# Kernel tuning notes

Measured on AMD Instinct MI355X. Metric: run time of the kernel, lower is better.

Reference implementation:

```python
import jax, jax.numpy as jnp
import numpy as np

N_NODES = 50000
N_GRAPHS = 64


def gcn_conv(x, W, b, src, dst, n_nodes):
    # PyG GCNConv: add self-loops, symmetric normalization D^-1/2 A D^-1/2,
    # linear transform, scatter-sum aggregation from src -> dst, plus bias.
    si = jnp.arange(n_nodes, dtype=src.dtype)
    s = jnp.concatenate([src, si])
    d = jnp.concatenate([dst, si])
    deg = jax.ops.segment_sum(jnp.ones_like(d, dtype=x.dtype), d, num_segments=n_nodes)
    dinv = jax.lax.rsqrt(jnp.maximum(deg, 1.0))  # deg >= 1 due to self-loops
    norm = dinv[s] * dinv[d]                      # [E+N]
    h = x @ W                                     # [N, out]
    msg = h[s] * norm[:, None]                    # gather + scale
    out = jax.ops.segment_sum(msg, d, num_segments=n_nodes)
    return out + b


def setup_inputs() -> dict:
    key = jax.random.key(0)
    ks = jax.random.split(key, 12)
    input_dim, hidden, half = 128, 64, 32
    x = jax.random.normal(ks[0], (N_NODES, input_dim), dtype=jnp.float32)
    edge_index = jax.random.randint(ks[1], (2, 800000), 0, N_NODES, dtype=jnp.int64)
    batch = jnp.sort(jax.random.randint(ks[2], (N_NODES,), 0, N_GRAPHS, dtype=jnp.int64))
    def lin(k, fan_in, fan_out):
        s = 1.0 / np.sqrt(fan_in)
        return jax.random.uniform(k, (fan_in, fan_out), jnp.float32, -s, s)
    return {
        "x": x,
        "edge_index": edge_index,
        "batch": batch,
        "W1": lin(ks[3], input_dim, hidden), "b1": jnp.zeros((hidden,), jnp.float32),
        "W2": lin(ks[4], hidden, hidden),    "b2": jnp.zeros((hidden,), jnp.float32),
        "Wc1": lin(ks[5], hidden, half),     "bc1": jnp.zeros((half,), jnp.float32),
        "Wc2": lin(ks[6], half, 1),          "bc2": jnp.zeros((1,), jnp.float32),
    }


def reference(x, edge_index, batch, W1, b1, W2, b2, Wc1, bc1, Wc2, bc2):
    src, dst = edge_index[0], edge_index[1]
    h = jax.nn.relu(gcn_conv(x, W1, b1, src, dst, N_NODES))
    # F.dropout(training=False) -> identity in eval
    h = jax.nn.relu(gcn_conv(h, W2, b2, src, dst, N_NODES))
    # global_mean_pool over graphs
    sums = jax.ops.segment_sum(h, batch, num_segments=N_GRAPHS)
    cnts = jax.ops.segment_sum(jnp.ones((h.shape[0], 1), h.dtype), batch, num_segments=N_GRAPHS)
    g = sums / jnp.maximum(cnts, 1.0)             # [G, hidden]
    # MLP head (Dropout(0.2) is identity in eval)
    z = jax.nn.relu(g @ Wc1 + bc1)
    return z @ Wc2 + bc2                          # [G, 1]
```

## Files before the change

### kernel.cpp

```cpp
#include <hip/hip_runtime.h>
#include <math.h>

#define NG 64
#define HID 64

typedef __attribute__((ext_vector_type(8))) short bf16x8;
typedef __attribute__((ext_vector_type(4))) float f32x4;

__device__ __forceinline__ unsigned int bfbits(float f) {
    unsigned int u = __float_as_uint(f);
    return (u + 0x7FFFu + ((u >> 16) & 1u)) >> 16;
}
__device__ __forceinline__ float bfval(unsigned int bits) {
    return __uint_as_float(bits << 16);
}

__global__ void k_deg(const int* __restrict__ dst, int E,
                      int* __restrict__ deg, int* __restrict__ rank) {
    int i = blockIdx.x * blockDim.x + threadIdx.x;
    if (i < E) rank[i] = atomicAdd(deg + dst[i], 1);
}

__global__ __launch_bounds__(256) void k_scan1(const int* __restrict__ deg,
                                               int* __restrict__ excl,
                                               int* __restrict__ bsum,
                                               float* __restrict__ dinv, int n) {
    __shared__ int tmp[256];
    int b = blockIdx.x, t = threadIdx.x;
    int base = b * 1024 + t * 4;
    int v[4];
#pragma unroll
    for (int j = 0; j < 4; ++j) v[j] = (base + j < n) ? deg[base + j] : 0;
#pragma unroll
    for (int j = 0; j < 4; ++j)
        if (base + j < n) dinv[base + j] = 1.0f / sqrtf((float)v[j] + 1.0f);
    int s = v[0] + v[1] + v[2] + v[3];
    tmp[t] = s;
    __syncthreads();
    for (int off = 1; off < 256; off <<= 1) {
        int x = (t >= off) ? tmp[t - off] : 0;
        __syncthreads();
        tmp[t] += x;
        __syncthreads();
    }
    int run = tmp[t] - s;
#pragma unroll
    for (int j = 0; j < 4; ++j) {
        if (base + j < n) excl[base + j] = run;
        run += v[j];
    }
    if (t == 255) bsum[b] = tmp[255];
}

__global__ __launch_bounds__(256) void k_scan23(const int* __restrict__ excl,
                                                const int* __restrict__ bsum,
                                                const int* __restrict__ batch,
                                                int* __restrict__ rowstart,
                                                int* __restrict__ gstart,
                                                int n, int E, int nb) {
    __shared__ int bs[256];
    __shared__ int pre;
    const int t = threadIdx.x;
    if (t < nb) bs[t] = bsum[t];
    __syncthreads();
    if (t == 0) {
        int seg = (blockIdx.x * 256) >> 10;
        int s = 0;
        for (int b = 0; b < seg; ++b) s += bs[b];
        pre = s;
    }
    __syncthreads();
    int i = blockIdx.x * 256 + t;
    if (i < n) {
        rowstart[i] = excl[i] + pre;
        int bi = batch[i];
        int bp = (i == 0) ? -1 : batch[i - 1];
        for (int g = bp + 1; g <= bi; ++g) gstart[g] = i;
        if (i == n - 1)
            for (int g = bi + 1; g <= NG; ++g) gstart[g] = n;
    }
    if (i == 0) rowstart[n] = E;
}

__global__ void k_fill(const int* __restrict__ src, const int* __restrict__ dst,
                       const int* __restrict__ rank, const int* __restrict__ rowstart,
                       int* __restrict__ col, int E) {
    int e = blockIdx.x * blockDim.x + threadIdx.x;
    if (e >= E) return;
    col[rowstart[dst[e]] + rank[e]] = src[e];
}

__global__ void k_wconv(const float* __restrict__ W1, const float* __restrict__ W2,
                        unsigned short* __restrict__ W1hi, unsigned short* __restrict__ W1lo,
                        unsigned short* __restrict__ W2hi, unsigned short* __restrict__ W2lo) {
    int i = blockIdx.x * blockDim.x + threadIdx.x;
    if (i < 128 * 64) {
        int k = i >> 6, c = i & 63;
        float f = W1[i];
        unsigned hb = bfbits(f);
        W1hi[c * 128 + k] = (unsigned short)hb;
        W1lo[c * 128 + k] = (unsigned short)bfbits(f - bfval(hb));
    }
    int i2 = i - 128 * 64;
    if (i2 >= 0 && i2 < 64 * 64) {
        int k = i2 >> 6, c = i2 & 63;
        float f = W2[i2];
        unsigned hb = bfbits(f);
        W2hi[c * 64 + k] = (unsigned short)hb;
        W2lo[c * 64 + k] = (unsigned short)bfbits(f - bfval(hb));
    }
}

template<int K>
__global__ __launch_bounds__(256) void k_gemm_mfma(const float* __restrict__ A,
                                                   const unsigned short* __restrict__ Whi,
                                                   const unsigned short* __restrict__ Wlo,
                                                   const float* __restrict__ dinv,
                                                   float* __restrict__ out, int n) {
    const int wave = threadIdx.x >> 6, lane = threadIdx.x & 63;
    const int ntile2 = (n + 31) >> 5;
    const int tile2 = blockIdx.x * 4 + wave;
    if (tile2 >= ntile2) return;
    const int lrow = lane & 15;
    const int kgrp = lane >> 4;
    const int r0 = tile2 * 32 + lrow;
    const int r1 = r0 + 16;

    f32x4 acc0[4], acc1[4];
#pragma unroll
    for (int ct = 0; ct < 4; ++ct) {
        acc0[ct] = (f32x4){0.f, 0.f, 0.f, 0.f};
        acc1[ct] = (f32x4){0.f, 0.f, 0.f, 0.f};
    }

#pragma unroll
    for (int s = 0; s < K / 32; ++s) {
        float a0[8], a1[8];
        {
            const float* p0 = A + (size_t)r0 * K + s * 32 + kgrp * 8;
            const float* p1 = A + (size_t)r1 * K + s * 32 + kgrp * 8;
            float4 u0, u1, w0, w1;
            if (r0 < n) { u0 = *(const float4*)p0; u1 = *(const float4*)(p0 + 4); }
            else { u0 = make_float4(0.f,0.f,0.f,0.f); u1 = u0; }
            if (r1 < n) { w0 = *(const float4*)p1; w1 = *(const float4*)(p1 + 4); }
            else { w0 = make_float4(0.f,0.f,0.f,0.f); w1 = w0; }
            a0[0]=u0.x; a0[1]=u0.y; a0[2]=u0.z; a0[3]=u0.w;
            a0[4]=u1.x; a0[5]=u1.y; a0[6]=u1.z; a0[7]=u1.w;
            a1[0]=w0.x; a1[1]=w0.y; a1[2]=w0.z; a1[3]=w0.w;
            a1[4]=w1.x; a1[5]=w1.y; a1[6]=w1.z; a1[7]=w1.w;
        }
        bf16x8 ahi0, alo0, ahi1, alo1;
#pragma unroll
        for (int e = 0; e < 8; ++e) {
            unsigned hb0 = bfbits(a0[e]);
            ahi0[e] = (short)hb0;
            alo0[e] = (short)bfbits(a0[e] - bfval(hb0));
            unsigned hb1 = bfbits(a1[e]);
            ahi1[e] = (short)hb1;
            alo1[e] = (short)bfbits(a1[e] - bfval(hb1));
        }
#pragma unroll
        for (int ct = 0; ct < 4; ++ct) {
            const size_t wo = (size_t)(ct * 16 + lrow) * K + s * 32 + kgrp * 8;
            bf16x8 whi = *(const bf16x8*)(Whi + wo);
            bf16x8 wlo = *(const bf16x8*)(Wlo + wo);
            acc0[ct] = __builtin_amdgcn_mfma_f32_16x16x32_bf16(ahi0, whi, acc0[ct], 0, 0, 0);
            acc0[ct] = __builtin_amdgcn_mfma_f32_16x16x32_bf16(alo0, whi, acc0[ct], 0, 0, 0);
            acc0[ct] = __builtin_amdgcn_mfma_f32_16x16x32_bf16(ahi0, wlo, acc0[ct], 0, 0, 0);
            acc1[ct] = __builtin_amdgcn_mfma_f32_16x16x32_bf16(ahi1, whi, acc1[ct], 0, 0, 0);
            acc1[ct] = __builtin_amdgcn_mfma_f32_16x16x32_bf16(alo1, whi, acc1[ct], 0, 0, 0);
            acc1[ct] = __builtin_amdgcn_mfma_f32_16x16x32_bf16(ahi1, wlo, acc1[ct], 0, 0, 0);
        }
    }

#pragma unroll
    for (int r = 0; r < 4; ++r) {
        int o0 = tile2 * 32 + kgrp * 4 + r;
        if (o0 < n) {
            float dv = dinv[o0];
#pragma unroll
            for (int ct = 0; ct < 4; ++ct)
                out[(size_t)o0 * HID + ct * 16 + lrow] = acc0[ct][r] * dv;
        }
        int o1 = o0 + 16;
        if (o1 < n) {
            float dv = dinv[o1];
#pragma unroll
            for (int ct = 0; ct < 4; ++ct)
                out[(size_t)o1 * HID + ct * 16 + lrow] = acc1[ct][r] * dv;
        }
    }
}

__global__ __launch_bounds__(256) void k_gather(const float* __restrict__ hs,
                                                const int* __restrict__ rowstart,
                                                const int* __restrict__ col,
                                                const float* __restrict__ dinv,
                                                const float* __restrict__ bias,
                                                float* __restrict__ out, int n) {
    const int wave = threadIdx.x >> 6, lane = threadIdx.x & 63;
    const int n0 = blockIdx.x * 8 + wave * 2;
    if (n0 >= n) return;
    const int n1 = n0 + 1;
    const bool has1 = (n1 < n);
    const float bl = bias[lane];

    float di0 = dinv[n0];
    float acc0 = hs[(size_t)n0 * HID + lane], acc0b = 0.f;
    int j0 = rowstart[n0], e0 = rowstart[n0 + 1];
    float di1 = 0.f, acc1 = 0.f, acc1b = 0.f;
    int j1 = 0, e1 = 0;
    if (has1) {
        di1 = dinv[n1];
        acc1 = hs[(size_t)n1 * HID + lane];
        j1 = e0;
        e1 = rowstart[n1 + 1];
    }

    while (e0 - j0 >= 8 && e1 - j1 >= 8) {
        const int jb0 = __builtin_amdgcn_readfirstlane(j0);
        const int jb1 = __builtin_amdgcn_readfirstlane(j1);
        int c0[8], c1[8];
#pragma unroll
        for (int t = 0; t < 8; ++t) c0[t] = col[jb0 + t];
#pragma unroll
        for (int t = 0; t < 8; ++t) c1[t] = col[jb1 + t];
        float v0[8], v1[8];
#pragma unroll
        for (int t = 0; t < 8; ++t) v0[t] = hs[(size_t)c0[t] * HID + lane];
#pragma unroll
        for (int t = 0; t < 8; ++t) v1[t] = hs[(size_t)c1[t] * HID + lane];
#pragma unroll
        for (int t = 0; t < 8; ++t) { if (t & 1) acc0b += v0[t]; else acc0 += v0[t]; }
#pragma unroll
        for (int t = 0; t < 8; ++t) { if (t & 1) acc1b += v1[t]; else acc1 += v1[t]; }
        j0 += 8; j1 += 8;
    }
    while (e0 - j0 >= 8) {
        const int jb = __builtin_amdgcn_readfirstlane(j0);
        int c[8];
#pragma unroll
        for (int t = 0; t < 8; ++t) c[t] = col[jb + t];
        float v[8];
#pragma unroll
        for (int t = 0; t < 8; ++t) v[t] = hs[(size_t)c[t] * HID + lane];
#pragma unroll
        for (int t = 0; t < 8; ++t) { if (t & 1) acc0b += v[t]; else acc0 += v[t]; }
        j0 += 8;
    }
    while (e1 - j1 >= 8) {
        const int jb = __builtin_amdgcn_readfirstlane(j1);
        int c[8];
#pragma unroll
        for (int t = 0; t < 8; ++t) c[t] = col[jb + t];
        float v[8];
#pragma unroll
        for (int t = 0; t < 8; ++t) v[t] = hs[(size_t)c[t] * HID + lane];
#pragma unroll
        for (int t = 0; t < 8; ++t) { if (t & 1) acc1b += v[t]; else acc1 += v[t]; }
        j1 += 8;
    }
    for (; j0 + 1 < e0; j0 += 2) {
        acc0  += hs[(size_t)col[j0] * HID + lane];
        acc0b += hs[(size_t)col[j0 + 1] * HID + lane];
    }
    if (j0 < e0) acc0 += hs[(size_t)col[j0] * HID + lane];
    for (; j1 + 1 < e1; j1 += 2) {
        acc1  += hs[(size_t)col[j1] * HID + lane];
        acc1b += hs[(size_t)col[j1 + 1] * HID + lane];
    }
    if (j1 < e1) acc1 += hs[(size_t)col[j1] * HID + lane];

    out[(size_t)n0 * HID + lane] = fmaxf(fmaf(acc0 + acc0b, di0, bl), 0.f);
    if (has1)
        out[(size_t)n1 * HID + lane] = fmaxf(fmaf(acc1 + acc1b, di1, bl), 0.f);
}

__global__ __launch_bounds__(512) void k_poolhead(const float* __restrict__ h,
                                                  const int* __restrict__ gstart,
                                                  const float* __restrict__ Wc1,
                                                  const float* __restrict__ bc1,
                                                  const float* __restrict__ Wc2,
                                                  const float* __restrict__ bc2,
                                                  float* __restrict__ outp, int n) {
    const int g = blockIdx.x;
    const int lo = gstart[g], lo2 = gstart[g + 1];
    const int t = threadIdx.x;
    const int rg = t >> 4;
    const int c4 = (t & 15) * 4;
    float4 acc = make_float4(0.f, 0.f, 0.f, 0.f);
    for (int r = lo + rg; r < lo2; r += 32) {
        float4 v = *(const float4*)(h + (size_t)r * HID + c4);
        acc.x += v.x; acc.y += v.y; acc.z += v.z; acc.w += v.w;
    }
    __shared__ float4 red[32][16];
    __shared__ float gmv[HID];
    __shared__ float zs[32];
    red[rg][t & 15] = acc;
    __syncthreads();
    if (t < 16) {
        float4 s = red[0][t];
#pragma unroll
        for (int g2 = 1; g2 < 32; ++g2) {
            float4 v = red[g2][t];
            s.x += v.x; s.y += v.y; s.z += v.z; s.w += v.w;
        }
        float inv = 1.0f / fmaxf((float)(lo2 - lo), 1.0f);
        gmv[t * 4 + 0] = s.x * inv; gmv[t * 4 + 1] = s.y * inv;
        gmv[t * 4 + 2] = s.z * inv; gmv[t * 4 + 3] = s.w * inv;
    }
    __syncthreads();
    if (t < 32) {
        float z = bc1[t];
#pragma unroll 8
        for (int k = 0; k < HID; ++k) z = fmaf(gmv[k], Wc1[k * 32 + t], z);
        zs[t] = fmaxf(z, 0.f) * Wc2[t];
    }
    __syncthreads();
    if (t == 0) {
        float o = bc2[0];
#pragma unroll
        for (int j = 0; j < 32; ++j) o += zs[j];
        outp[g] = o;
    }
}

extern "C" void kernel_launch(void* const* d_in, const int* in_sizes, int n_in,
                              void* d_out, int out_size, void* d_ws, size_t ws_size,
                              hipStream_t stream) {
    const float* x    = (const float*)d_in[0];
    const int*   ei   = (const int*)d_in[1];
    const int*   batch= (const int*)d_in[2];
    const float* W1   = (const float*)d_in[3];
    const float* b1   = (const float*)d_in[4];
    const float* W2   = (const float*)d_in[5];
    const float* b2   = (const float*)d_in[6];
    const float* Wc1  = (const float*)d_in[7];
    const float* bc1  = (const float*)d_in[8];
    const float* Wc2  = (const float*)d_in[9];
    const float* bc2  = (const float*)d_in[10];

    const int E = in_sizes[1] / 2;
    const int n = in_sizes[0] / 128;
    const int* srcp = ei;
    const int* dstp = ei + E;
    const int nb = (n + 1023) / 1024;

    char* ws = (char*)d_ws;
    auto alloc = [&](size_t bytes) {
        char* p = ws;
        ws += (bytes + 255) & ~(size_t)255;
        return p;
    };
    int*   deg      = (int*)  alloc((size_t)n * 4);
    float* dinv     = (float*)alloc((size_t)n * 4);
    int*   excl     = (int*)  alloc((size_t)n * 4);
    int*   bsum     = (int*)  alloc((size_t)nb * 4);
    int*   rowstart = (int*)  alloc((size_t)(n + 1) * 4);
    int*   gstart   = (int*)  alloc((size_t)(NG + 1) * 4);
    int*   rank     = (int*)  alloc((size_t)E * 4);
    int*   col      = (int*)  alloc((size_t)E * 4);
    float* bufA     = (float*)alloc((size_t)n * HID * 4);
    float* bufB     = (float*)alloc((size_t)n * HID * 4);
    unsigned short* W1hi = (unsigned short*)alloc(128 * 64 * 2);
    unsigned short* W1lo = (unsigned short*)alloc(128 * 64 * 2);
    unsigned short* W2hi = (unsigned short*)alloc(64 * 64 * 2);
    unsigned short* W2lo = (unsigned short*)alloc(64 * 64 * 2);

    hipMemsetAsync(deg, 0, (size_t)n * 4, stream);

    k_deg   <<<(E + 255) / 256, 256, 0, stream>>>(dstp, E, deg, rank);
    k_scan1 <<<nb, 256, 0, stream>>>(deg, excl, bsum, dinv, n);
    k_scan23<<<(n + 255) / 256, 256, 0, stream>>>(excl, bsum, batch, rowstart, gstart, n, E, nb);
    k_fill  <<<(E + 255) / 256, 256, 0, stream>>>(srcp, dstp, rank, rowstart, col, E);
    k_wconv <<<(128 * 64 + 64 * 64 + 255) / 256, 256, 0, stream>>>(W1, W2, W1hi, W1lo, W2hi, W2lo);

    const int mblocks = ((n + 31) / 32 + 3) / 4;
    const int gblocks = (n + 7) / 8;

    k_gemm_mfma<128><<<mblocks, 256, 0, stream>>>(x, W1hi, W1lo, dinv, bufA, n);
    k_gather<<<gblocks, 256, 0, stream>>>(bufA, rowstart, col, dinv, b1, bufB, n);

    k_gemm_mfma<64><<<mblocks, 256, 0, stream>>>(bufB, W2hi, W2lo, dinv, bufA, n);
    k_gather<<<gblocks, 256, 0, stream>>>(bufA, rowstart, col, dinv, b2, bufB, n);

    k_poolhead<<<NG, 512, 0, stream>>>(bufB, gstart, Wc1, bc1, Wc2, bc2, (float*)d_out, n);
}
```

Baseline: 169.9 us.

## Fuse layer-1 gather with layer-2 GEMM and merge weight conversion into scan

Adds a kernel that aggregates 32 nodes per block into shared memory, applies bias and ReLU, then runs the 64x64 layer-2 transform with split-bf16 MFMA and dinv scaling directly. This removes one launch and a full N×64 intermediate write and read. The weight hi/lo conversion now runs as extra blocks of the scan23 kernel, removing one more launch. The fused kernel uses 512-thread blocks with a barrier between gather and GEMM, which may reduce latency hiding for the irregular gathers.

```diff
diff --git a/kernel.cpp b/kernel.cpp
--- a/kernel.cpp
+++ b/kernel.cpp
@@ -57,10 +57,34 @@
                                                 const int* __restrict__ batch,
                                                 int* __restrict__ rowstart,
                                                 int* __restrict__ gstart,
-                                                int n, int E, int nb) {
+                                                const float* __restrict__ W1,
+                                                const float* __restrict__ W2,
+                                                unsigned short* __restrict__ W1hi,
+                                                unsigned short* __restrict__ W1lo,
+                                                unsigned short* __restrict__ W2hi,
+                                                unsigned short* __restrict__ W2lo,
+                                                int n, int E, int nb, int nblk) {
+    const int t = threadIdx.x;
+    if (blockIdx.x >= nblk) {
+        int idx = (blockIdx.x - nblk) * 256 + t;
+        if (idx < 128 * 64) {
+            int k = idx >> 6, c = idx & 63;
+            float f = W1[idx];
+            unsigned hb = bfbits(f);
+            W1hi[c * 128 + k] = (unsigned short)hb;
+            W1lo[c * 128 + k] = (unsigned short)bfbits(f - bfval(hb));
+        } else if (idx < 128 * 64 + 64 * 64) {
+            int i2 = idx - 128 * 64;
+            int k = i2 >> 6, c = i2 & 63;
+            float f = W2[i2];
+            unsigned hb = bfbits(f);
+            W2hi[c * 64 + k] = (unsigned short)hb;
+            W2lo[c * 64 + k] = (unsigned short)bfbits(f - bfval(hb));
+        }
+        return;
+    }
     __shared__ int bs[256];
     __shared__ int pre;
-    const int t = threadIdx.x;
     if (t < nb) bs[t] = bsum[t];
     __syncthreads();
     if (t == 0) {
@@ -88,27 +112,6 @@
     int e = blockIdx.x * blockDim.x + threadIdx.x;
     if (e >= E) return;
     col[rowstart[dst[e]] + rank[e]] = src[e];
-}
-
-__global__ void k_wconv(const float* __restrict__ W1, const float* __restrict__ W2,
-                        unsigned short* __restrict__ W1hi, unsigned short* __restrict__ W1lo,
-                        unsigned short* __restrict__ W2hi, unsigned short* __restrict__ W2lo) {
-    int i = blockIdx.x * blockDim.x + threadIdx.x;
-    if (i < 128 * 64) {
-        int k = i >> 6, c = i & 63;
-        float f = W1[i];
-        unsigned hb = bfbits(f);
-        W1hi[c * 128 + k] = (unsigned short)hb;
-        W1lo[c * 128 + k] = (unsigned short)bfbits(f - bfval(hb));
-    }
-    int i2 = i - 128 * 64;
-    if (i2 >= 0 && i2 < 64 * 64) {
-        int k = i2 >> 6, c = i2 & 63;
-        float f = W2[i2];
-        unsigned hb = bfbits(f);
-        W2hi[c * 64 + k] = (unsigned short)hb;
-        W2lo[c * 64 + k] = (unsigned short)bfbits(f - bfval(hb));
-    }
 }
 
 template<int K>
@@ -192,6 +195,128 @@
     }
 }
 
+__global__ __launch_bounds__(512) void k_gather_gemm2(const float* __restrict__ hs,
+                                                      const int* __restrict__ rowstart,
+                                                      const int* __restrict__ col,
+                                                      const float* __restrict__ dinv,
+                                                      const float* __restrict__ bias,
+                                                      const unsigned short* __restrict__ Whi,
+                                                      const unsigned short* __restrict__ Wlo,
+                                                      float* __restrict__ outB, int n) {
+    __shared__ float Ash[32][68];
+    const int wave = threadIdx.x >> 6, lane = threadIdx.x & 63;
+    const int nodebase = blockIdx.x * 32 + wave * 4;
+    const float bl = bias[lane];
+
+#pragma unroll
+    for (int p = 0; p < 2; ++p) {
+        const int n0 = nodebase + 2 * p;
+        const int n1 = n0 + 1;
+        const bool has0 = (n0 < n), has1 = (n1 < n);
+        float di0 = 0.f, acc0 = 0.f, acc0b = 0.f;
+        float di1 = 0.f, acc1 = 0.f, acc1b = 0.f;
+        int j0 = 0, e0 = 0, j1 = 0, e1 = 0;
+        if (has0) {
+            di0 = dinv[n0];
+            acc0 = hs[(size_t)n0 * HID + lane];
+            j0 = rowstart[n0]; e0 = rowstart[n0 + 1];
+        }
+        if (has1) {
+            di1 = dinv[n1];
+            acc1 = hs[(size_t)n1 * HID + lane];
+            j1 = e0; e1 = rowstart[n1 + 1];
+        }
+        while (e0 - j0 >= 8 && e1 - j1 >= 8) {
+            const int jb0 = __builtin_amdgcn_readfirstlane(j0);
+            const int jb1 = __builtin_amdgcn_readfirstlane(j1);
+            int c0[8], c1[8];
+#pragma unroll
+            for (int t = 0; t < 8; ++t) c0[t] = col[jb0 + t];
+#pragma unroll
+            for (int t = 0; t < 8; ++t) c1[t] = col[jb1 + t];
+            float v0[8], v1[8];
+#pragma unroll
+            for (int t = 0; t < 8; ++t) v0[t] = hs[(size_t)c0[t] * HID + lane];
+#pragma unroll
+            for (int t = 0; t < 8; ++t) v1[t] = hs[(size_t)c1[t] * HID + lane];
+#pragma unroll
+            for (int t = 0; t < 8; ++t) { if (t & 1) acc0b += v0[t]; else acc0 += v0[t]; }
+#pragma unroll
+            for (int t = 0; t < 8; ++t) { if (t & 1) acc1b += v1[t]; else acc1 += v1[t]; }
+            j0 += 8; j1 += 8;
+        }
+        while (e0 - j0 >= 8) {
+            const int jb = __builtin_amdgcn_readfirstlane(j0);
+            int c[8];
+#pragma unroll
+            for (int t = 0; t < 8; ++t) c[t] = col[jb + t];
+            float v[8];
+#pragma unroll
+            for (int t = 0; t < 8; ++t) v[t] = hs[(size_t)c[t] * HID + lane];
+#pragma unroll
+            for (int t = 0; t < 8; ++t) { if (t & 1) acc0b += v[t]; else acc0 += v[t]; }
+            j0 += 8;
+        }
+        while (e1 - j1 >= 8) {
+            const int jb = __builtin_amdgcn_readfirstlane(j1);
+            int c[8];
+#pragma unroll
+            for (int t = 0; t < 8; ++t) c[t] = col[jb + t];
+            float v[8];
+#pragma unroll
+            for (int t = 0; t < 8; ++t) v[t] = hs[(size_t)c[t] * HID + lane];
+#pragma unroll
+            for (int t = 0; t < 8; ++t) { if (t & 1) acc1b += v[t]; else acc1 += v[t]; }
+            j1 += 8;
+        }
+        for (; j0 + 1 < e0; j0 += 2) {
+            acc0  += hs[(size_t)col[j0] * HID + lane];
+            acc0b += hs[(size_t)col[j0 + 1] * HID + lane];
+        }
+        if (j0 < e0) acc0 += hs[(size_t)col[j0] * HID + lane];
+        for (; j1 + 1 < e1; j1 += 2) {
+            acc1  += hs[(size_t)col[j1] * HID + lane];
+            acc1b += hs[(size_t)col[j1 + 1] * HID + lane];
+        }
+        if (j1 < e1) acc1 += hs[(size_t)col[j1] * HID + lane];
+
+        Ash[wave * 4 + 2 * p][lane]     = has0 ? fmaxf(fmaf(acc0 + acc0b, di0, bl), 0.f) : 0.f;
+        Ash[wave * 4 + 2 * p + 1][lane] = has1 ? fmaxf(fmaf(acc1 + acc1b, di1, bl), 0.f) : 0.f;
+    }
+    __syncthreads();
+
+    const int rowhalf = wave >> 2, ct = wave & 3;
+    const int lrow = lane & 15;
+    const int kgrp = lane >> 4;
+    f32x4 acc = (f32x4){0.f, 0.f, 0.f, 0.f};
+#pragma unroll
+    for (int s = 0; s < 2; ++s) {
+        const float* ap = &Ash[rowhalf * 16 + lrow][s * 32 + kgrp * 8];
+        float4 u0 = *(const float4*)ap;
+        float4 u1 = *(const float4*)(ap + 4);
+        float av[8] = {u0.x, u0.y, u0.z, u0.w, u1.x, u1.y, u1.z, u1.w};
+        bf16x8 ahi, alo;
+#pragma unroll
+        for (int e = 0; e < 8; ++e) {
+            unsigned hb = bfbits(av[e]);
+            ahi[e] = (short)hb;
+            alo[e] = (short)bfbits(av[e] - bfval(hb));
+        }
+        const size_t wo = (size_t)(ct * 16 + lrow) * 64 + s * 32 + kgrp * 8;
+        bf16x8 whi = *(const bf16x8*)(Whi + wo);
+        bf16x8 wlo = *(const bf16x8*)(Wlo + wo);
+        acc = __builtin_amdgcn_mfma_f32_16x16x32_bf16(ahi, whi, acc, 0, 0, 0);
+        acc = __builtin_amdgcn_mfma_f32_16x16x32_bf16(alo, whi, acc, 0, 0, 0);
+        acc = __builtin_amdgcn_mfma_f32_16x16x32_bf16(ahi, wlo, acc, 0, 0, 0);
+    }
+#pragma unroll
+    for (int r = 0; r < 4; ++r) {
+        int orow = blockIdx.x * 32 + rowhalf * 16 + kgrp * 4 + r;
+        if (orow < n)
+            outB[(size_t)orow * HID + ct * 16 + lrow] = acc[r] * dinv[orow];
+    }
+}
+
 __global__ __launch_bounds__(256) void k_gather(const float* __restrict__ hs,
                                                 const int* __restrict__ rowstart,
                                                 const int* __restrict__ col,
@@ -213,10 +338,8 @@
     if (has1) {
         di1 = dinv[n1];
         acc1 = hs[(size_t)n1 * HID + lane];
-        j1 = e0;
-        e1 = rowstart[n1 + 1];
-    }
-
+        j1 = e0; e1 = rowstart[n1 + 1];
+    }
     while (e0 - j0 >= 8 && e1 - j1 >= 8) {
         const int jb0 = __builtin_amdgcn_readfirstlane(j0);
         const int jb1 = __builtin_amdgcn_readfirstlane(j1);
@@ -369,20 +492,22 @@
 
     hipMemsetAsync(deg, 0, (size_t)n * 4, stream);
 
+    const int nblk = (n + 255) / 256;
+    const int wblk = (128 * 64 + 64 * 64 + 255) / 256;
+
     k_deg   <<<(E + 255) / 256, 256, 0, stream>>>(dstp, E, deg, rank);
     k_scan1 <<<nb, 256, 0, stream>>>(deg, excl, bsum, dinv, n);
-    k_scan23<<<(n + 255) / 256, 256, 0, stream>>>(excl, bsum, batch, rowstart, gstart, n, E, nb);
+    k_scan23<<<nblk + wblk, 256, 0, stream>>>(excl, bsum, batch, rowstart, gstart,
+                                              W1, W2, W1hi, W1lo, W2hi, W2lo,
+                                              n, E, nb, nblk);
     k_fill  <<<(E + 255) / 256, 256, 0, stream>>>(srcp, dstp, rank, rowstart, col, E);
-    k_wconv <<<(128 * 64 + 64 * 64 + 255) / 256, 256, 0, stream>>>(W1, W2, W1hi, W1lo, W2hi, W2lo);
 
     const int mblocks = ((n + 31) / 32 + 3) / 4;
-    const int gblocks = (n + 7) / 8;
 
     k_gemm_mfma<128><<<mblocks, 256, 0, stream>>>(x, W1hi, W1lo, dinv, bufA, n);
-    k_gather<<<gblocks, 256, 0, stream>>>(bufA, rowstart, col, dinv, b1, bufB, n);
-
-    k_gemm_mfma<64><<<mblocks, 256, 0, stream>>>(bufB, W2hi, W2lo, dinv, bufA, n);
-    k_gather<<<gblocks, 256, 0, stream>>>(bufA, rowstart, col, dinv, b2, bufB, n);
-
-    k_poolhead<<<NG, 512, 0, stream>>>(bufB, gstart, Wc1, bc1, Wc2, bc2, (float*)d_out, n);
-}
+    k_gather_gemm2<<<(n + 31) / 32, 512, 0, stream>>>(bufA, rowstart, col, dinv, b1,
+                                                      W2hi, W2lo, bufB, n);
+    k_gather<<<(n + 7) / 8, 256, 0, stream>>>(bufB, rowstart, col, dinv, b2, bufA, n);
+
+    k_poolhead<<<NG, 512, 0, stream>>>(bufA, gstart, Wc1, bc1, Wc2, bc2, (float*)d_out, n);
+}
```

New measurement: 162.6 us. 4.3% less time.
